# Kernel optimization log

Measured on AMD Instinct MI355X. Metric: run time of the kernel, lower is better.

## Reference

```python
import jax, jax.numpy as jnp
import numpy as np

B, L, D, H = 4, 2048, 1024, 16
HD = D // H


def setup_inputs() -> dict:
    key = jax.random.key(0)
    k1, k2, k3 = jax.random.split(key, 3)
    # xavier_uniform bounds for Linear(d, 3d) and Linear(d, d)
    b_qkv = float(np.sqrt(6.0 / (D + 3 * D)))
    b_out = float(np.sqrt(6.0 / (D + D)))
    x = jax.random.normal(k1, (B, L, D), dtype=jnp.float32)
    W_qkv = jax.random.uniform(k2, (3 * D, D), dtype=jnp.float32, minval=-b_qkv, maxval=b_qkv)
    W_out = jax.random.uniform(k3, (D, D), dtype=jnp.float32, minval=-b_out, maxval=b_out)
    return {"x": x, "W_qkv": W_qkv, "W_out": W_out}


def reference(x, W_qkv, W_out):
    b, l, d = x.shape
    # fused QKV projection: [B,L,3d] -> [3,B,H,L,Hd]
    qkv = (x @ W_qkv.T).reshape(b, l, 3, H, HD).transpose(2, 0, 3, 1, 4)
    q, k, v = qkv[0], qkv[1], qkv[2]
    # naive causal attention: full [B,H,L,L] score matrix, as in the original
    scores = jnp.einsum('bhqd,bhkd->bhqk', q, k) / (HD ** 0.5)
    mask = jnp.tril(jnp.ones((l, l), dtype=bool))  # causal mask recomputed per call
    scores = jnp.where(mask, scores, -jnp.inf)
    attn = jax.nn.softmax(scores, axis=-1)
    ctx = jnp.einsum('bhqk,bhkd->bhqd', attn, v)          # [B,H,L,Hd]
    ctx = ctx.transpose(0, 2, 1, 3).reshape(b, l, d)       # [B,L,d]
    return ctx @ W_out.T
```

## Files before the change

### kernel.cpp

```cpp
#include <hip/hip_runtime.h>

#define BB 4
#define LL 2048
#define DD 1024
#define HH 16
#define HD 64

typedef __attribute__((ext_vector_type(8))) short s16x8;
typedef __attribute__((ext_vector_type(4))) short s16x4;
typedef __attribute__((ext_vector_type(4))) float f32x4;

#define SCALE_LOG2E 0.18033688011112042f

__device__ __forceinline__ short f2bf(float f) {
  union { float f; unsigned u; } c;
  c.f = f;
  return (short)((c.u + 0x7fffu + ((c.u >> 16) & 1u)) >> 16);
}

__device__ __forceinline__ void cp16(const void* g, void* l) {
  __builtin_amdgcn_global_load_lds(
      (const __attribute__((address_space(1))) void*)g,
      (__attribute__((address_space(3))) void*)l, 16, 0, 0);
}

__global__ __launch_bounds__(256) void f2b_kernel(const float* __restrict__ in,
                                                  short* __restrict__ out, int n4) {
  int i = blockIdx.x * blockDim.x + threadIdx.x;
  if (i >= n4) return;
  float4 v = ((const float4*)in)[i];
  s16x4 o;
  o[0] = f2bf(v.x);
  o[1] = f2bf(v.y);
  o[2] = f2bf(v.z);
  o[3] = f2bf(v.w);
  ((s16x4*)out)[i] = o;
}

template <int MODE>
__global__ __launch_bounds__(256) void gemm_bt(const short* __restrict__ A,
                                               const short* __restrict__ Bm,
                                               int K, int N,
                                               short* __restrict__ qo,
                                               short* __restrict__ ko,
                                               short* __restrict__ vo,
                                               float* __restrict__ fo) {
  __shared__ __align__(16) short As[2][128 * 32];
  __shared__ __align__(16) short Bs[2][128 * 32];
  const int tid = threadIdx.x;
  const int m0 = blockIdx.y * 128, n0 = blockIdx.x * 128;
  const int wave = tid >> 6, lane = tid & 63;
  const int quad = lane >> 4, c16 = lane & 15;
  const int wr = (wave >> 1) * 64, wc = (wave & 1) * 64;

  f32x4 zero = {0.f, 0.f, 0.f, 0.f};
  f32x4 acc[4][4];
#pragma unroll
  for (int i = 0; i < 4; i++)
#pragma unroll
    for (int j = 0; j < 4; j++) acc[i][j] = zero;

  const int row1 = tid >> 2, seg = (tid & 3) * 8;
  const short* Ag = A + (size_t)(m0 + row1) * K + seg;
  const short* Bg = Bm + (size_t)(n0 + row1) * K + seg;

  auto stage = [&](int k0, int bi) {
    cp16(Ag + k0, As[bi] + wave * 512);
    cp16(Ag + (size_t)64 * K + k0, As[bi] + 2048 + wave * 512);
    cp16(Bg + k0, Bs[bi] + wave * 512);
    cp16(Bg + (size_t)64 * K + k0, Bs[bi] + 2048 + wave * 512);
  };

  stage(0, 0);
  __syncthreads();
  const int T = K >> 5;
  for (int t = 0; t < T; t++) {
    if (t + 1 < T) stage((t + 1) * 32, (t + 1) & 1);
    const short* Asb = As[t & 1];
    const short* Bsb = Bs[t & 1];
    s16x8 af[4], bf[4];
#pragma unroll
    for (int i = 0; i < 4; i++)
      af[i] = *(const s16x8*)&Asb[(wr + i * 16 + c16) * 32 + quad * 8];
#pragma unroll
    for (int j = 0; j < 4; j++)
      bf[j] = *(const s16x8*)&Bsb[(wc + j * 16 + c16) * 32 + quad * 8];
#pragma unroll
    for (int i = 0; i < 4; i++)
#pragma unroll
      for (int j = 0; j < 4; j++)
        acc[i][j] = __builtin_amdgcn_mfma_f32_16x16x32_bf16(af[i], bf[j], acc[i][j], 0, 0, 0);
    __syncthreads();
  }

  if (MODE == 0) {
#pragma unroll
    for (int j = 0; j < 4; j++) {
      const int gn = n0 + wc + j * 16 + c16;
      const int which = gn >> 10;
      const int h = (gn >> 6) & 15;
      const int hd = gn & 63;
      if (which == 2) {
#pragma unroll
        for (int i = 0; i < 4; i++) {
          const int gm = m0 + wr + i * 16 + quad * 4;
          const int b = gm >> 11, l = gm & 2047;
          s16x4 vv;
#pragma unroll
          for (int r = 0; r < 4; r++) vv[r] = f2bf(acc[i][j][r]);
          *(s16x4*)&vo[((size_t)((b << 4) + h) * HD + hd) * LL + l] = vv;
        }
      } else {
        short* dst = which == 0 ? qo : ko;
        const float sc = which == 0 ? SCALE_LOG2E : 1.0f;
#pragma unroll
        for (int i = 0; i < 4; i++)
#pragma unroll
          for (int r = 0; r < 4; r++) {
            const int gm = m0 + wr + i * 16 + quad * 4 + r;
            const int b = gm >> 11, l = gm & 2047;
            dst[((size_t)((b << 4) + h) * LL + l) * HD + hd] = f2bf(acc[i][j][r] * sc);
          }
      }
    }
  } else {
#pragma unroll
    for (int i = 0; i < 4; i++)
#pragma unroll
      for (int r = 0; r < 4; r++) {
        const int gm = m0 + wr + i * 16 + quad * 4 + r;
#pragma unroll
        for (int j = 0; j < 4; j++) {
          const int gn = n0 + wc + j * 16 + c16;
          fo[(size_t)gm * N + gn] = acc[i][j][r];
        }
      }
  }
}

__global__ __launch_bounds__(512, 4) void attn_kernel(const short* __restrict__ Qb,
                                                      const short* __restrict__ Kb,
                                                      const short* __restrict__ Vtb,
                                                      short* __restrict__ Cb) {
  const int pi = blockIdx.x;
  const int bh = blockIdx.y;
  const int tid = threadIdx.x;
  const int wave = tid >> 6, lane = tid & 63;
  const int quad = lane >> 4, c16 = lane & 15;
  const int sw = c16 & 7;
  const size_t base = (size_t)bh * LL * HD;
  const short* Q = Qb + base;
  const short* K = Kb + base;
  const short* Vt = Vtb + base;

  __shared__ __align__(16) short Ks[2][128 * 64];
  __shared__ __align__(16) short Vs[2][64 * 128];

  const f32x4 zero = {0.f, 0.f, 0.f, 0.f};
  const s16x4 ones = {(short)0x3F80, (short)0x3F80, (short)0x3F80, (short)0x3F80};

  const int k_r = lane >> 3, k_c = lane & 7;
  const int v_r = lane >> 4, v_c = lane & 15;
  const int ksw = (k_c ^ k_r) * 8;
  const int vsw = (v_c ^ ((wave * 4 + v_r) & 15)) * 8;
  auto stage = [&](int kb, int bi) {
#pragma unroll
    for (int i = 0; i < 2; i++) {
      const int gk = i * 64 + wave * 8 + k_r;
      cp16(K + (size_t)(kb + gk) * HD + ksw, &Ks[bi][(i * 64 + wave * 8) * 64]);
      const int gv = i * 32 + wave * 4 + v_r;
      cp16(Vt + (size_t)gv * LL + kb + vsw, &Vs[bi][(i * 32 + wave * 4) * 128]);
    }
  };

  auto pack4 = [&](const float* p) {
    union { float f; unsigned u; } a0, a1, a2, a3;
    a0.f = p[0]; a1.f = p[1]; a2.f = p[2]; a3.f = p[3];
    union { s16x4 v; unsigned u[2]; } r;
    r.u[0] = __builtin_amdgcn_perm(a1.u, a0.u, 0x07060302u);
    r.u[1] = __builtin_amdgcn_perm(a3.u, a2.u, 0x07060302u);
    return r.v;
  };

  for (int phase = 0; phase < 2; phase++) {
    const int qg = phase == 0 ? (15 - pi) : pi;
    const int qw = qg * 128 + wave * 16;
    const int tiles = qg + 1;

    s16x8 qf[2];
#pragma unroll
    for (int s = 0; s < 2; s++)
      qf[s] = *(const s16x8*)(Q + (size_t)(qw + c16) * HD + s * 32 + quad * 8);

    f32x4 o[4];
#pragma unroll
    for (int j4 = 0; j4 < 4; j4++) o[j4] = zero;
    f32x4 ol = zero;

    stage(0, 0);
    __syncthreads();

    for (int t = 0; t < tiles; t++) {
      const int kb = t * 128;
      if (t + 1 < tiles) stage(kb + 128, (t + 1) & 1);
      const short* Kt = &Ks[t & 1][0];
      const short* Vv = &Vs[t & 1][0];

      const int D = qw - kb;
      const int jm = min((D >> 4) + 1, 8);
      const int jb = D >> 4;

#pragma unroll
      for (int j = 0; j < 8; j++) {
        if (j >= jm) continue;
        s16x8 kf0 = *(const s16x8*)&Kt[(j * 16 + c16) * 64 + ((quad ^ sw) * 8)];
        s16x8 kf1 = *(const s16x8*)&Kt[(j * 16 + c16) * 64 + (((4 + quad) ^ sw) * 8)];
        s16x4 va[4];
#pragma unroll
        for (int j4 = 0; j4 < 4; j4++)
          va[j4] = *(const s16x4*)&Vv[(j4 * 16 + c16) * 128 +
                                      (((2 * j + (quad >> 1)) ^ c16) * 8) + (quad & 1) * 4];
        f32x4 s = __builtin_amdgcn_mfma_f32_16x16x32_bf16(kf0, qf[0], zero, 0, 0, 0);
        s = __builtin_amdgcn_mfma_f32_16x16x32_bf16(kf1, qf[1], s, 0, 0, 0);
        float p[4];
#pragma unroll
        for (int r = 0; r < 4; r++) p[r] = __builtin_amdgcn_exp2f(s[r]);
        if (j == jb) {
          const int thr = c16 + D - j * 16 - quad * 4;
#pragma unroll
          for (int r = 0; r < 4; r++)
            if (r > thr) p[r] = 0.f;
        }
        s16x4 pb = pack4(p);
        ol = __builtin_amdgcn_mfma_f32_16x16x16bf16_1k(ones, pb, ol, 0, 0, 0);
#pragma unroll
        for (int j4 = 0; j4 < 4; j4++)
          o[j4] = __builtin_amdgcn_mfma_f32_16x16x16bf16_1k(va[j4], pb, o[j4], 0, 0, 0);
      }

      __syncthreads();
    }

    const int b = bh >> 4, h2 = bh & 15;
    const float inv = 1.0f / ol[0];
    const int q = qw + c16;
#pragma unroll
    for (int j4 = 0; j4 < 4; j4++) {
      s16x4 ov;
#pragma unroll
      for (int r = 0; r < 4; r++) ov[r] = f2bf(o[j4][r] * inv);
      *(s16x4*)&Cb[(size_t)(b * LL + q) * DD + h2 * HD + j4 * 16 + quad * 4] = ov;
    }
  }
}

extern "C" void kernel_launch(void* const* d_in, const int* in_sizes, int n_in,
                              void* d_out, int out_size, void* d_ws, size_t ws_size,
                              hipStream_t stream) {
  const float* x = (const float*)d_in[0];
  const float* wqkv = (const float*)d_in[1];
  const float* wout = (const float*)d_in[2];
  float* out = (float*)d_out;

  const size_t NX = (size_t)BB * LL * DD;
  short* xb = (short*)d_ws;
  short* wqkvb = xb + NX;
  short* woutb = wqkvb + (size_t)3 * DD * DD;
  short* qb = woutb + (size_t)DD * DD;
  short* kb = qb + NX;
  short* vb = kb + NX;
  short* cb = vb + NX;

  f2b_kernel<<<dim3((unsigned)(NX / 4 / 256)), 256, 0, stream>>>(x, xb, (int)(NX / 4));
  f2b_kernel<<<dim3(3 * DD * DD / 4 / 256), 256, 0, stream>>>(wqkv, wqkvb, 3 * DD * DD / 4);
  f2b_kernel<<<dim3(DD * DD / 4 / 256), 256, 0, stream>>>(wout, woutb, DD * DD / 4);

  gemm_bt<0><<<dim3(3 * DD / 128, BB * LL / 128), 256, 0, stream>>>(
      xb, wqkvb, DD, 3 * DD, qb, kb, vb, nullptr);
  attn_kernel<<<dim3(8, BB * HH), 512, 0, stream>>>(qb, kb, vb, cb);
  gemm_bt<1><<<dim3(DD / 128, BB * LL / 128), 256, 0, stream>>>(
      cb, woutb, DD, DD, nullptr, nullptr, nullptr, out);
}
```

Before: 253.0 us.

## Deepen GEMM LDS pipeline to four stages with XOR swizzle and prio hints

```diff
diff --git a/kernel.cpp b/kernel.cpp
--- a/kernel.cpp
+++ b/kernel.cpp
@@ -45,8 +45,8 @@
                                                short* __restrict__ ko,
                                                short* __restrict__ vo,
                                                float* __restrict__ fo) {
-  __shared__ __align__(16) short As[2][128 * 32];
-  __shared__ __align__(16) short Bs[2][128 * 32];
+  __shared__ __align__(16) short As[4][128 * 32];
+  __shared__ __align__(16) short Bs[4][128 * 32];
   const int tid = threadIdx.x;
   const int m0 = blockIdx.y * 128, n0 = blockIdx.x * 128;
   const int wave = tid >> 6, lane = tid & 63;
@@ -60,37 +60,51 @@
 #pragma unroll
     for (int j = 0; j < 4; j++) acc[i][j] = zero;
 
-  const int row1 = tid >> 2, seg = (tid & 3) * 8;
-  const short* Ag = A + (size_t)(m0 + row1) * K + seg;
-  const short* Bg = Bm + (size_t)(n0 + row1) * K + seg;
-
-  auto stage = [&](int k0, int bi) {
+  const int row1 = tid >> 2;
+  const int gsw = ((tid & 3) ^ ((tid >> 3) & 3)) * 8;
+  const short* Ag = A + (size_t)(m0 + row1) * K + gsw;
+  const short* Bg = Bm + (size_t)(n0 + row1) * K + gsw;
+  const int rsw = (quad ^ ((c16 >> 1) & 3)) * 8;
+
+  auto stage = [&](int t) {
+    const int bi = t & 3, k0 = t << 5;
     cp16(Ag + k0, As[bi] + wave * 512);
     cp16(Ag + (size_t)64 * K + k0, As[bi] + 2048 + wave * 512);
     cp16(Bg + k0, Bs[bi] + wave * 512);
     cp16(Bg + (size_t)64 * K + k0, Bs[bi] + 2048 + wave * 512);
   };
 
-  stage(0, 0);
-  __syncthreads();
   const int T = K >> 5;
+  stage(0);
+  stage(1);
+  stage(2);
+  asm volatile("s_waitcnt vmcnt(8)" ::: "memory");
+  __builtin_amdgcn_s_barrier();
+  asm volatile("" ::: "memory");
+
   for (int t = 0; t < T; t++) {
-    if (t + 1 < T) stage((t + 1) * 32, (t + 1) & 1);
-    const short* Asb = As[t & 1];
-    const short* Bsb = Bs[t & 1];
-    s16x8 af[4], bf[4];
+    const short* Asb = As[t & 3];
+    const short* Bsb = Bs[t & 3];
+    s16x8 af[4], bfv[4];
 #pragma unroll
     for (int i = 0; i < 4; i++)
-      af[i] = *(const s16x8*)&Asb[(wr + i * 16 + c16) * 32 + quad * 8];
+      af[i] = *(const s16x8*)&Asb[(wr + i * 16 + c16) * 32 + rsw];
 #pragma unroll
     for (int j = 0; j < 4; j++)
-      bf[j] = *(const s16x8*)&Bsb[(wc + j * 16 + c16) * 32 + quad * 8];
+      bfv[j] = *(const s16x8*)&Bsb[(wc + j * 16 + c16) * 32 + rsw];
+    if (t + 3 < T) stage(t + 3);
+    __builtin_amdgcn_s_setprio(1);
 #pragma unroll
     for (int i = 0; i < 4; i++)
 #pragma unroll
       for (int j = 0; j < 4; j++)
-        acc[i][j] = __builtin_amdgcn_mfma_f32_16x16x32_bf16(af[i], bf[j], acc[i][j], 0, 0, 0);
-    __syncthreads();
+        acc[i][j] = __builtin_amdgcn_mfma_f32_16x16x32_bf16(af[i], bfv[j], acc[i][j], 0, 0, 0);
+    __builtin_amdgcn_s_setprio(0);
+    if (t < T - 3) asm volatile("s_waitcnt vmcnt(8)" ::: "memory");
+    else if (t == T - 3) asm volatile("s_waitcnt vmcnt(4)" ::: "memory");
+    else if (t == T - 2) asm volatile("s_waitcnt vmcnt(0)" ::: "memory");
+    __builtin_amdgcn_s_barrier();
+    asm volatile("" ::: "memory");
   }
 
   if (MODE == 0) {
```

New measurement: 250.8 us. About the same (-0.9%).

## Replace GEMM with 8-wave, larger-tile, swizzled, ping-pong pipelined kernel

Applied to the files above, without the earlier changes.

```diff
diff --git a/kernel.cpp b/kernel.cpp
--- a/kernel.cpp
+++ b/kernel.cpp
@@ -23,6 +23,21 @@
       (const __attribute__((address_space(1))) void*)g,
       (__attribute__((address_space(3))) void*)l, 16, 0, 0);
 }
+
+template <int N>
+__device__ __forceinline__ void waitvm() {
+  static_assert(N == 0 || N == 3 || N == 4, "vmcnt imm");
+  if constexpr (N == 0) asm volatile("s_waitcnt vmcnt(0)" ::: "memory");
+  else if constexpr (N == 3) asm volatile("s_waitcnt vmcnt(3)" ::: "memory");
+  else if constexpr (N == 4) asm volatile("s_waitcnt vmcnt(4)" ::: "memory");
+}
+
+#define BAR()                                  \
+  do {                                         \
+    asm volatile("" ::: "memory");             \
+    __builtin_amdgcn_s_barrier();              \
+    asm volatile("" ::: "memory");             \
+  } while (0)
 
 __global__ __launch_bounds__(256) void f2b_kernel(const float* __restrict__ in,
                                                   short* __restrict__ out, int n4) {
@@ -37,60 +52,141 @@
   ((s16x4*)out)[i] = o;
 }
 
-template <int MODE>
-__global__ __launch_bounds__(256) void gemm_bt(const short* __restrict__ A,
-                                               const short* __restrict__ Bm,
-                                               int K, int N,
-                                               short* __restrict__ qo,
-                                               short* __restrict__ ko,
-                                               short* __restrict__ vo,
-                                               float* __restrict__ fo) {
-  __shared__ __align__(16) short As[2][128 * 32];
-  __shared__ __align__(16) short Bs[2][128 * 32];
+template <int BM, int MODE>
+__global__ __launch_bounds__(512, 2) void gemm8(const short* __restrict__ A,
+                                                const short* __restrict__ Bm,
+                                                int K, int N,
+                                                short* __restrict__ qo,
+                                                short* __restrict__ ko,
+                                                short* __restrict__ vo,
+                                                float* __restrict__ fo) {
+  constexpr int MR = BM / 32;
+  constexpr int LA = BM / 128;
+  constexpr int VM = LA + 2;
+
+  __shared__ __align__(16) short As[2][2][BM * 32];
+  __shared__ __align__(16) short Bs[2][2][256 * 32];
   const int tid = threadIdx.x;
-  const int m0 = blockIdx.y * 128, n0 = blockIdx.x * 128;
+  const int m0 = blockIdx.y * BM, n0 = blockIdx.x * 256;
   const int wave = tid >> 6, lane = tid & 63;
   const int quad = lane >> 4, c16 = lane & 15;
-  const int wr = (wave >> 1) * 64, wc = (wave & 1) * 64;
+  const int wr = (wave >> 2) * (BM / 2), wc = (wave & 3) * 64;
 
   f32x4 zero = {0.f, 0.f, 0.f, 0.f};
-  f32x4 acc[4][4];
-#pragma unroll
-  for (int i = 0; i < 4; i++)
+  f32x4 acc[MR][4];
+#pragma unroll
+  for (int i = 0; i < MR; i++)
 #pragma unroll
     for (int j = 0; j < 4; j++) acc[i][j] = zero;
 
-  const int row1 = tid >> 2, seg = (tid & 3) * 8;
-  const short* Ag = A + (size_t)(m0 + row1) * K + seg;
-  const short* Bg = Bm + (size_t)(n0 + row1) * K + seg;
-
-  auto stage = [&](int k0, int bi) {
-    cp16(Ag + k0, As[bi] + wave * 512);
-    cp16(Ag + (size_t)64 * K + k0, As[bi] + 2048 + wave * 512);
-    cp16(Bg + k0, Bs[bi] + wave * 512);
-    cp16(Bg + (size_t)64 * K + k0, Bs[bi] + 2048 + wave * 512);
-  };
-
-  stage(0, 0);
-  __syncthreads();
-  const int T = K >> 5;
-  for (int t = 0; t < T; t++) {
-    if (t + 1 < T) stage((t + 1) * 32, (t + 1) & 1);
-    const short* Asb = As[t & 1];
-    const short* Bsb = Bs[t & 1];
-    s16x8 af[4], bf[4];
-#pragma unroll
-    for (int i = 0; i < 4; i++)
-      af[i] = *(const s16x8*)&Asb[(wr + i * 16 + c16) * 32 + quad * 8];
-#pragma unroll
-    for (int j = 0; j < 4; j++)
-      bf[j] = *(const s16x8*)&Bsb[(wc + j * 16 + c16) * 32 + quad * 8];
-#pragma unroll
-    for (int i = 0; i < 4; i++)
-#pragma unroll
-      for (int j = 0; j < 4; j++)
-        acc[i][j] = __builtin_amdgcn_mfma_f32_16x16x32_bf16(af[i], bf[j], acc[i][j], 0, 0, 0);
-    __syncthreads();
+  const int srow = wave * 16 + (lane >> 2);
+  const int gsw = ((lane & 3) ^ ((lane >> 3) & 3)) * 8;
+  const short* Ag = A + (size_t)(m0 + srow) * K + gsw;
+  const short* Bg = Bm + (size_t)(n0 + srow) * K + gsw;
+  const int rsw = (quad ^ ((c16 >> 1) & 3)) * 8;
+
+  auto stageA = [&](int t, int s) {
+    const int bi = t & 1, k0 = t * 64 + s * 32;
+#pragma unroll
+    for (int i = 0; i < LA; i++)
+      cp16(Ag + (size_t)(i * 128) * K + k0, &As[bi][s][(i * 128 + wave * 16) * 32]);
+  };
+  auto stageB = [&](int t, int s) {
+    const int bi = t & 1, k0 = t * 64 + s * 32;
+#pragma unroll
+    for (int i = 0; i < 2; i++)
+      cp16(Bg + (size_t)(i * 128) * K + k0, &Bs[bi][s][(i * 128 + wave * 16) * 32]);
+  };
+
+  s16x8 af[MR];
+  auto rdA = [&](int bi, int s) {
+#pragma unroll
+    for (int i = 0; i < MR; i++)
+      af[i] = *(const s16x8*)&As[bi][s][(wr + i * 16 + c16) * 32 + rsw];
+  };
+  auto rdB = [&](int bi, int s, int j) {
+    return *(const s16x8*)&Bs[bi][s][(wc + j * 16 + c16) * 32 + rsw];
+  };
+  auto mm2 = [&](s16x8 b0, s16x8 b1, int c) {
+    __builtin_amdgcn_s_setprio(1);
+#pragma unroll
+    for (int i = 0; i < MR; i++) {
+      acc[i][2 * c] = __builtin_amdgcn_mfma_f32_16x16x32_bf16(af[i], b0, acc[i][2 * c], 0, 0, 0);
+      acc[i][2 * c + 1] =
+          __builtin_amdgcn_mfma_f32_16x16x32_bf16(af[i], b1, acc[i][2 * c + 1], 0, 0, 0);
+    }
+    __builtin_amdgcn_s_setprio(0);
+  };
+
+  stageA(0, 0);
+  stageB(0, 0);
+  stageA(0, 1);
+  stageB(0, 1);
+  waitvm<VM>();
+  BAR();
+
+  const int J = K >> 7;
+  for (int j = 0; j < J; j++) {
+    const bool last = (j == J - 1);
+    const int to = 2 * j + 1, te = 2 * j + 2;
+    s16x8 b0, b1;
+    rdA(0, 0);
+    b0 = rdB(0, 0, 0);
+    b1 = rdB(0, 0, 1);
+    stageA(to, 0);
+    BAR();
+    mm2(b0, b1, 0);
+    BAR();
+    b0 = rdB(0, 0, 2);
+    b1 = rdB(0, 0, 3);
+    stageB(to, 0);
+    BAR();
+    mm2(b0, b1, 1);
+    waitvm<VM>();
+    BAR();
+    rdA(0, 1);
+    b0 = rdB(0, 1, 0);
+    b1 = rdB(0, 1, 1);
+    stageA(to, 1);
+    BAR();
+    mm2(b0, b1, 0);
+    BAR();
+    b0 = rdB(0, 1, 2);
+    b1 = rdB(0, 1, 3);
+    stageB(to, 1);
+    BAR();
+    mm2(b0, b1, 1);
+    waitvm<VM>();
+    BAR();
+    rdA(1, 0);
+    b0 = rdB(1, 0, 0);
+    b1 = rdB(1, 0, 1);
+    if (!last) stageA(te, 0);
+    BAR();
+    mm2(b0, b1, 0);
+    BAR();
+    b0 = rdB(1, 0, 2);
+    b1 = rdB(1, 0, 3);
+    if (!last) stageB(te, 0);
+    BAR();
+    mm2(b0, b1, 1);
+    if (last) waitvm<0>();
+    else waitvm<VM>();
+    BAR();
+    rdA(1, 1);
+    b0 = rdB(1, 1, 0);
+    b1 = rdB(1, 1, 1);
+    if (!last) stageA(te, 1);
+    BAR();
+    mm2(b0, b1, 0);
+    BAR();
+    b0 = rdB(1, 1, 2);
+    b1 = rdB(1, 1, 3);
+    if (!last) stageB(te, 1);
+    BAR();
+    mm2(b0, b1, 1);
+    if (!last) waitvm<VM>();
+    BAR();
   }
 
   if (MODE == 0) {
@@ -102,7 +198,7 @@
       const int hd = gn & 63;
       if (which == 2) {
 #pragma unroll
-        for (int i = 0; i < 4; i++) {
+        for (int i = 0; i < MR; i++) {
           const int gm = m0 + wr + i * 16 + quad * 4;
           const int b = gm >> 11, l = gm & 2047;
           s16x4 vv;
@@ -114,7 +210,7 @@
         short* dst = which == 0 ? qo : ko;
         const float sc = which == 0 ? SCALE_LOG2E : 1.0f;
 #pragma unroll
-        for (int i = 0; i < 4; i++)
+        for (int i = 0; i < MR; i++)
 #pragma unroll
           for (int r = 0; r < 4; r++) {
             const int gm = m0 + wr + i * 16 + quad * 4 + r;
@@ -125,7 +221,7 @@
     }
   } else {
 #pragma unroll
-    for (int i = 0; i < 4; i++)
+    for (int i = 0; i < MR; i++)
 #pragma unroll
       for (int r = 0; r < 4; r++) {
         const int gm = m0 + wr + i * 16 + quad * 4 + r;
@@ -275,9 +371,9 @@
   f2b_kernel<<<dim3(3 * DD * DD / 4 / 256), 256, 0, stream>>>(wqkv, wqkvb, 3 * DD * DD / 4);
   f2b_kernel<<<dim3(DD * DD / 4 / 256), 256, 0, stream>>>(wout, woutb, DD * DD / 4);
 
-  gemm_bt<0><<<dim3(3 * DD / 128, BB * LL / 128), 256, 0, stream>>>(
+  gemm8<256, 0><<<dim3(3 * DD / 256, BB * LL / 256), 512, 0, stream>>>(
       xb, wqkvb, DD, 3 * DD, qb, kb, vb, nullptr);
   attn_kernel<<<dim3(8, BB * HH), 512, 0, stream>>>(qb, kb, vb, cb);
-  gemm_bt<1><<<dim3(DD / 128, BB * LL / 128), 256, 0, stream>>>(
+  gemm8<128, 1><<<dim3(DD / 256, BB * LL / 128), 512, 0, stream>>>(
       cb, woutb, DD, DD, nullptr, nullptr, nullptr, out);
 }
```

After: 266.4 us. 5.3% more time.
